# Kernel tuning notes

Hardware: AMD Instinct MI355X
Metric: run time of the kernel (lower is better)

## Reference

```python
import jax, jax.numpy as jnp
import numpy as np

N_NODES = 50000
N_EDGES = 800000
D_NODE = 128
D_EDGE = 16
HID = 128
BN_EPS = 1e-5


def gcn_conv(h, src, dst, W, b):
    # PyG GCNConv: h' = D^-1/2 (A + I) D^-1/2 (h W) + b, deg includes self-loop
    h = h @ W
    deg = jax.ops.segment_sum(jnp.ones((src.shape[0],), h.dtype), dst,
                              num_segments=N_NODES) + 1.0
    dinv = deg ** -0.5
    norm = dinv[src] * dinv[dst]                      # [E]
    agg = jax.ops.segment_sum(h[src] * norm[:, None], dst,
                              num_segments=N_NODES)   # scatter to dst
    agg = agg + h * (dinv * dinv)[:, None]            # self-loop term
    return agg + b


def setup_inputs() -> dict:
    key = jax.random.key(0)
    ks = jax.random.split(key, 12)
    s = lambda fan_in: 1.0 / np.sqrt(fan_in)
    return {
        "x": jax.random.normal(ks[0], (N_NODES, D_NODE), jnp.float32),
        "edge_index": jax.random.randint(ks[1], (2, N_EDGES), 0, N_NODES, jnp.int32),
        "edge_attr": jax.random.normal(ks[2], (N_EDGES, D_EDGE), jnp.float32),
        "W1": jax.random.normal(ks[3], (D_NODE, HID), jnp.float32) * s(D_NODE),
        "b1": jnp.zeros((HID,), jnp.float32),
        "gamma": jnp.ones((HID,), jnp.float32),
        "beta": jnp.zeros((HID,), jnp.float32),
        "W2": jax.random.normal(ks[4], (HID, HID), jnp.float32) * s(HID),
        "b2": jnp.zeros((HID,), jnp.float32),
        "Wm1": jax.random.normal(ks[5], (2 * HID + D_EDGE, HID), jnp.float32) * s(2 * HID + D_EDGE),
        "bm1": jnp.zeros((HID,), jnp.float32),
        "Wm2": jax.random.normal(ks[6], (HID, 1), jnp.float32) * s(HID),
        "bm2": jnp.zeros((1,), jnp.float32),
    }


def reference(x, edge_index, edge_attr, W1, b1, gamma, beta, W2, b2, Wm1, bm1, Wm2, bm2):
    src, dst = edge_index[0], edge_index[1]
    z = gcn_conv(x, src, dst, W1, b1)
    # BatchNorm1d over nodes (training-mode batch stats, biased var)
    mean = jnp.mean(z, axis=0)
    var = jnp.mean(jnp.square(z - mean), axis=0)
    z = (z - mean) * jax.lax.rsqrt(var + BN_EPS) * gamma + beta
    z = jax.nn.relu(z)
    z = gcn_conv(z, src, dst, W2, b2)
    # edge head: gather endpoints, concat with edge_attr, 2-layer MLP (dropout = eval identity)
    edge_input = jnp.concatenate([z[src], z[dst], edge_attr], axis=1)  # [E, 2H+De]
    h = jax.nn.relu(edge_input @ Wm1 + bm1)
    return (h @ Wm2 + bm2).squeeze(-1)  # [E]
```

## Files before the change

kernel.cpp:

```cpp
#include <hip/hip_runtime.h>
#include <hip/hip_bf16.h>

#define NN 50000
#define NE 800000
#define H 128
#define DE 16
#define BN_EPS 1e-5f
#define NB_SCAN 196

typedef float v2f __attribute__((ext_vector_type(2)));
typedef float v4f __attribute__((ext_vector_type(4)));
typedef short bfrag __attribute__((ext_vector_type(8)));

__device__ __forceinline__ unsigned int packbf2(float a, float b) {
    __hip_bfloat162 h = __float22bfloat162_rn(make_float2(a, b));
    return *(unsigned int*)&h;
}
__device__ __forceinline__ v2f unpackbf2(unsigned int u) {
    v2f r;
    r.x = __uint_as_float(u << 16);
    r.y = __uint_as_float(u & 0xffff0000u);
    return r;
}
__device__ __forceinline__ bfrag cvt8(float4 a0, float4 a1) {
    union { uint4 u; bfrag f; } x;
    x.u.x = packbf2(a0.x, a0.y);
    x.u.y = packbf2(a0.z, a0.w);
    x.u.z = packbf2(a1.x, a1.y);
    x.u.w = packbf2(a1.z, a1.w);
    return x.f;
}
__device__ __forceinline__ bfrag cvt8v(v4f a0, v4f a1) {
    union { uint4 u; bfrag f; } x;
    x.u.x = packbf2(a0.x, a0.y);
    x.u.y = packbf2(a0.z, a0.w);
    x.u.z = packbf2(a1.x, a1.y);
    x.u.w = packbf2(a1.z, a1.w);
    return x.f;
}
#define COMP(u4, j) ((j) == 0 ? (u4).x : (j) == 1 ? (u4).y : (j) == 2 ? (u4).z : (u4).w)

__global__ void hist_k(const int* __restrict__ dst, int* __restrict__ counts) {
    int e = blockIdx.x * 256 + threadIdx.x;
    if (e < NE) atomicAdd(&counts[dst[e]], 1);
}

__global__ void scan1_k(const int* __restrict__ counts, int* __restrict__ bsum) {
    __shared__ int sh[256];
    int i = blockIdx.x * 256 + threadIdx.x;
    int v = (i < NN) ? counts[i] : 0;
    sh[threadIdx.x] = v;
    __syncthreads();
    for (int off = 128; off; off >>= 1) {
        if (threadIdx.x < off) sh[threadIdx.x] += sh[threadIdx.x + off];
        __syncthreads();
    }
    if (!threadIdx.x) bsum[blockIdx.x] = sh[0];
}

__global__ void scan2_k(int* __restrict__ bsum) {
    __shared__ int sh[256];
    int t = threadIdx.x;
    int v = (t < NB_SCAN) ? bsum[t] : 0;
    sh[t] = v;
    __syncthreads();
    for (int off = 1; off < 256; off <<= 1) {
        int x = (t >= off) ? sh[t - off] : 0;
        __syncthreads();
        sh[t] += x;
        __syncthreads();
    }
    if (t < NB_SCAN) bsum[t] = sh[t] - v;
}

__global__ void scan3_k(const int* __restrict__ counts, const int* __restrict__ bsum,
                        int* __restrict__ offsets, int* __restrict__ cursor,
                        float* __restrict__ dinv) {
    __shared__ int sh[256];
    int i = blockIdx.x * 256 + threadIdx.x;
    int v = (i < NN) ? counts[i] : 0;
    sh[threadIdx.x] = v;
    __syncthreads();
    for (int off = 1; off < 256; off <<= 1) {
        int x = (threadIdx.x >= off) ? sh[threadIdx.x - off] : 0;
        __syncthreads();
        sh[threadIdx.x] += x;
        __syncthreads();
    }
    if (i < NN) {
        int excl = sh[threadIdx.x] - v + bsum[blockIdx.x];
        offsets[i] = excl;
        cursor[i] = excl;
        dinv[i] = rsqrtf((float)v + 1.0f);
    }
}

__global__ void fill_k(const int* __restrict__ src, const int* __restrict__ dst,
                       int* __restrict__ cursor, int* __restrict__ srcs) {
    int e = blockIdx.x * 256 + threadIdx.x;
    if (e < NE) {
        int d = dst[e];
        int pos = atomicAdd(&cursor[d], 1);
        srcs[pos] = src[e];
    }
}

__global__ void cvtB_k(const float* __restrict__ s0, const float* __restrict__ s1,
                       const float* __restrict__ s2, const float* __restrict__ s3,
                       short* __restrict__ d0, short* __restrict__ d1,
                       short* __restrict__ d2, short* __restrict__ d3) {
    const float* s = blockIdx.y == 0 ? s0 : blockIdx.y == 1 ? s1 : blockIdx.y == 2 ? s2 : s3;
    short* d = blockIdx.y == 0 ? d0 : blockIdx.y == 1 ? d1 : blockIdx.y == 2 ? d2 : d3;
    int idx = blockIdx.x * 256 + threadIdx.x;
    int n = idx & 127, k = idx >> 7;
    float v = s[k * 128 + n];
    d[n * 128 + k] = (short)(packbf2(v, v) & 0xffff);
}

__global__ void cvtWe_k(const float* __restrict__ We, unsigned int* __restrict__ WePk) {
    int idx = blockIdx.x * 256 + threadIdx.x;
    if (idx < 2048) {
        int c = idx >> 8;
        int lane = (idx >> 2) & 63;
        int j2 = (idx & 3) * 2;
        int q = lane >> 4, i = lane & 15;
        int k0 = q * 8 + j2, k1 = k0 + 1;
        int feat = i * 8 + c;
        float v0 = (k0 < 16) ? We[k0 * 128 + feat] : 0.f;
        float v1 = (k1 < 16) ? We[k1 * 128 + feat] : 0.f;
        WePk[idx] = packbf2(v0, v1);
    }
}

__global__ __launch_bounds__(256) void gemm_mfma(const float* __restrict__ A,
                                                 const short* __restrict__ Bt,
                                                 float* __restrict__ C,
                                                 unsigned int* __restrict__ Cb,
                                                 const float* __restrict__ rowScale,
                                                 const float* __restrict__ tA,
                                                 const float* __restrict__ tC,
                                                 int M) {
    int lane = threadIdx.x & 63;
    int w = threadIdx.x >> 6;
    int i = lane & 15;
    int q = lane >> 4;
    int r0 = blockIdx.x * 64 + w * 16;
    int arow = min(r0 + i, M - 1);
    const float* Arow = A + (size_t)arow * 128;

    v4f acc[8];
#pragma unroll
    for (int c = 0; c < 8; c++) acc[c] = (v4f)0.f;

#pragma unroll
    for (int kc = 0; kc < 128; kc += 32) {
        int kb = kc + q * 8;
        float4 a0 = *(const float4*)&Arow[kb];
        float4 a1 = *(const float4*)&Arow[kb + 4];
        if (tA) {
            float4 t0 = *(const float4*)&tA[kb];
            float4 t1 = *(const float4*)&tA[kb + 4];
            float4 c0 = *(const float4*)&tC[kb];
            float4 c1 = *(const float4*)&tC[kb + 4];
            a0.x = fmaxf(a0.x * t0.x + c0.x, 0.f);
            a0.y = fmaxf(a0.y * t0.y + c0.y, 0.f);
            a0.z = fmaxf(a0.z * t0.z + c0.z, 0.f);
            a0.w = fmaxf(a0.w * t0.w + c0.w, 0.f);
            a1.x = fmaxf(a1.x * t1.x + c1.x, 0.f);
            a1.y = fmaxf(a1.y * t1.y + c1.y, 0.f);
            a1.z = fmaxf(a1.z * t1.z + c1.z, 0.f);
            a1.w = fmaxf(a1.w * t1.w + c1.w, 0.f);
        }
        bfrag af = cvt8(a0, a1);
#pragma unroll
        for (int c = 0; c < 8; c++) {
            bfrag bf = *(const bfrag*)&Bt[(size_t)(c * 16 + i) * 128 + kb];
            acc[c] = __builtin_amdgcn_mfma_f32_16x16x32_bf16(af, bf, acc[c], 0, 0, 0);
        }
    }

    int orow0 = r0 + q * 4;
    v4f ds = (v4f)1.f;
    if (rowScale) ds = *(const v4f*)&rowScale[min(orow0, M - 4)];
    if (Cb) {
#pragma unroll
        for (int c = 0; c < 8; c++) {
            int col = c * 16 + i;
#pragma unroll
            for (int r = 0; r < 4; r++) {
                float v = acc[c][r] * ds[r];
                float vp = __shfl_xor(v, 1, 64);
                if (!(i & 1) && orow0 + r < M)
                    Cb[(size_t)(orow0 + r) * 64 + (col >> 1)] = packbf2(v, vp);
            }
        }
    } else {
#pragma unroll
        for (int c = 0; c < 8; c++) {
            int col = c * 16 + i;
#pragma unroll
            for (int r = 0; r < 4; r++) {
                if (orow0 + r < M)
                    C[(size_t)(orow0 + r) * 128 + col] = acc[c][r] * ds[r];
            }
        }
    }
}

__global__ __launch_bounds__(256) void gemm_pq(const unsigned int* __restrict__ zbA,
                                               const short* __restrict__ Bs_,
                                               const short* __restrict__ Bd_,
                                               const float* __restrict__ bm1,
                                               unsigned int* __restrict__ Pb,
                                               unsigned int* __restrict__ Qb,
                                               int M) {
    int lane = threadIdx.x & 63;
    int w = threadIdx.x >> 6;
    int i = lane & 15;
    int q = lane >> 4;
    int r0 = blockIdx.x * 64 + w * 16;
    int arow = min(r0 + i, M - 1);

    v4f accP[8], accQ[8];
#pragma unroll
    for (int c = 0; c < 8; c++) { accP[c] = (v4f)0.f; accQ[c] = (v4f)0.f; }

#pragma unroll
    for (int kc = 0; kc < 128; kc += 32) {
        int kb = kc + q * 8;
        bfrag af = *(const bfrag*)&zbA[(size_t)arow * 64 + (kb >> 1)];
#pragma unroll
        for (int c = 0; c < 8; c++) {
            bfrag bs = *(const bfrag*)&Bs_[(size_t)(c * 16 + i) * 128 + kb];
            bfrag bd = *(const bfrag*)&Bd_[(size_t)(c * 16 + i) * 128 + kb];
            accP[c] = __builtin_amdgcn_mfma_f32_16x16x32_bf16(af, bs, accP[c], 0, 0, 0);
            accQ[c] = __builtin_amdgcn_mfma_f32_16x16x32_bf16(af, bd, accQ[c], 0, 0, 0);
        }
    }

    int orow0 = r0 + q * 4;
    float bm1c[8];
#pragma unroll
    for (int c = 0; c < 8; c++) bm1c[c] = bm1[c * 16 + i];
#pragma unroll
    for (int c = 0; c < 8; c++) {
        int col = c * 16 + i;
#pragma unroll
        for (int r = 0; r < 4; r++) {
            float vP = accP[c][r];
            float vPp = __shfl_xor(vP, 1, 64);
            float vQ = accQ[c][r] + bm1c[c];
            float vQp = __shfl_xor(vQ, 1, 64);
            if (!(i & 1) && orow0 + r < M) {
                Pb[(size_t)(orow0 + r) * 64 + (col >> 1)] = packbf2(vP, vPp);
                Qb[(size_t)(orow0 + r) * 64 + (col >> 1)] = packbf2(vQ, vQp);
            }
        }
    }
}

__global__ __launch_bounds__(256, 8) void aggregate_k(const unsigned int* __restrict__ hsb,
                                                      const int* __restrict__ offsets,
                                                      const int* __restrict__ counts,
                                                      const int* __restrict__ srcs,
                                                      const float* __restrict__ dinv,
                                                      const float* __restrict__ bias,
                                                      float* __restrict__ zout,
                                                      unsigned int* __restrict__ zbout) {
    int lane = threadIdx.x & 63;
    int n = __builtin_amdgcn_readfirstlane(blockIdx.x * 4 + (threadIdx.x >> 6));
    if (n >= NN) return;
    int beg = offsets[n];
    int cnt = counts[n];
    v2f a0 = {0.f, 0.f}, a1 = {0.f, 0.f}, a2 = {0.f, 0.f}, a3 = {0.f, 0.f};
    v2f a4 = {0.f, 0.f}, a5 = {0.f, 0.f}, a6 = {0.f, 0.f}, a7 = {0.f, 0.f};
    for (int c = 0; c < cnt; c += 64) {
        int vsrc = srcs[beg + c + lane];
        int m = min(64, cnt - c);
        int t = 0;
        for (; t + 8 <= m; t += 8) {
            int s0 = __builtin_amdgcn_readlane(vsrc, t);
            int s1 = __builtin_amdgcn_readlane(vsrc, t + 1);
            int s2 = __builtin_amdgcn_readlane(vsrc, t + 2);
            int s3 = __builtin_amdgcn_readlane(vsrc, t + 3);
            int s4 = __builtin_amdgcn_readlane(vsrc, t + 4);
            int s5 = __builtin_amdgcn_readlane(vsrc, t + 5);
            int s6 = __builtin_amdgcn_readlane(vsrc, t + 6);
            int s7 = __builtin_amdgcn_readlane(vsrc, t + 7);
            unsigned int u0 = hsb[(size_t)s0 * 64 + lane];
            unsigned int u1 = hsb[(size_t)s1 * 64 + lane];
            unsigned int u2 = hsb[(size_t)s2 * 64 + lane];
            unsigned int u3 = hsb[(size_t)s3 * 64 + lane];
            unsigned int u4 = hsb[(size_t)s4 * 64 + lane];
            unsigned int u5 = hsb[(size_t)s5 * 64 + lane];
            unsigned int u6 = hsb[(size_t)s6 * 64 + lane];
            unsigned int u7 = hsb[(size_t)s7 * 64 + lane];
            a0 += unpackbf2(u0);
            a1 += unpackbf2(u1);
            a2 += unpackbf2(u2);
            a3 += unpackbf2(u3);
            a4 += unpackbf2(u4);
            a5 += unpackbf2(u5);
            a6 += unpackbf2(u6);
            a7 += unpackbf2(u7);
        }
        for (; t < m; t++) {
            int s0 = __builtin_amdgcn_readlane(vsrc, t);
            a0 += unpackbf2(hsb[(size_t)s0 * 64 + lane]);
        }
    }
    v2f self = unpackbf2(hsb[(size_t)n * 64 + lane]);
    float di = dinv[n];
    int f = lane * 2;
    float2 b = *(const float2*)&bias[f];
    v2f sum = ((a0 + a1) + (a2 + a3)) + ((a4 + a5) + (a6 + a7)) + self;
    float rx = sum.x * di + b.x;
    float ry = sum.y * di + b.y;
    if (zbout) {
        zbout[(size_t)n * 64 + lane] = packbf2(rx, ry);
    } else {
        *(float2*)&zout[(size_t)n * 128 + f] = make_float2(rx, ry);
    }
}

__global__ __launch_bounds__(256) void bnstats_k(const float* __restrict__ z,
                                                 float* __restrict__ sums,
                                                 float* __restrict__ sumsq) {
    __shared__ float ls[128], lq[128];
    int f = threadIdx.x & 127;
    int sub = threadIdx.x >> 7;
    float s = 0.f, q = 0.f;
    for (int r = blockIdx.x * 2 + sub; r < NN; r += gridDim.x * 2) {
        float v = z[(size_t)r * 128 + f];
        s += v;
        q += v * v;
    }
    if (sub) { ls[f] = s; lq[f] = q; }
    __syncthreads();
    if (!sub) {
        atomicAdd(&sums[f], s + ls[f]);
        atomicAdd(&sumsq[f], q + lq[f]);
    }
}

__global__ void bnfinal_k(const float* __restrict__ sums, const float* __restrict__ sumsq,
                          const float* __restrict__ gamma, const float* __restrict__ beta,
                          float* __restrict__ bnA, float* __restrict__ bnC) {
    int f = threadIdx.x;
    if (f < 128) {
        float mean = sums[f] * (1.0f / NN);
        float var = sumsq[f] * (1.0f / NN) - mean * mean;
        float a = gamma[f] * rsqrtf(var + BN_EPS);
        bnA[f] = a;
        bnC[f] = beta[f] - mean * a;
    }
}

__global__ __launch_bounds__(256) void edgehead_k(const unsigned int* __restrict__ Pb,
                                                  const unsigned int* __restrict__ Qb,
                                                  const float* __restrict__ ea,
                                                  const int* __restrict__ srcI,
                                                  const int* __restrict__ dstI,
                                                  const unsigned int* __restrict__ WePk,
                                                  const float* __restrict__ Wm2,
                                                  const float* __restrict__ bm2,
                                                  float* __restrict__ out) {
    int lane = threadIdx.x & 63;
    int wid = threadIdx.x >> 6;
    int base = (blockIdx.x * 4 + wid) * 64;
    int i = lane & 15;
    int q = lane >> 4;

    bfrag wef[8];
#pragma unroll
    for (int c = 0; c < 8; c++)
        wef[c] = *(const bfrag*)&WePk[(c * 64 + lane) * 4];
    float4 wv0 = *(const float4*)&Wm2[i * 8];
    float4 wv1 = *(const float4*)&Wm2[i * 8 + 4];
    float bm2v = bm2[0];

    int sv = srcI[base + lane];
    int dv = dstI[base + lane];

#pragma unroll
    for (int t = 0; t < 4; t++) {
        int tb = t * 16;
        bfrag af;
#pragma unroll
        for (int z = 0; z < 8; z++) af[z] = 0;
        if (q < 2) {
            const float* erow = &ea[(size_t)(base + tb + i) * 16 + q * 8];
            v4f e0 = __builtin_nontemporal_load((const v4f*)erow);
            v4f e1 = __builtin_nontemporal_load((const v4f*)(erow + 4));
            af = cvt8v(e0, e1);
        }
        uint4 Pu[4], Qu[4];
#pragma unroll
        for (int r = 0; r < 4; r++) {
            int sr = __shfl(sv, tb + q * 4 + r, 64);
            int dr = __shfl(dv, tb + q * 4 + r, 64);
            Pu[r] = *(const uint4*)&Pb[(size_t)sr * 64 + i * 4];
            Qu[r] = *(const uint4*)&Qb[(size_t)dr * 64 + i * 4];
        }
        v4f acc[8];
#pragma unroll
        for (int c = 0; c < 8; c++) acc[c] = (v4f)0.f;
#pragma unroll
        for (int c = 0; c < 8; c++)
            acc[c] = __builtin_amdgcn_mfma_f32_16x16x32_bf16(af, wef[c], acc[c], 0, 0, 0);
        float wvp[8] = {wv0.x, wv0.y, wv0.z, wv0.w, wv1.x, wv1.y, wv1.z, wv1.w};
#pragma unroll
        for (int r = 0; r < 4; r++) {
            float s = 0.f;
#pragma unroll
            for (int j = 0; j < 4; j++) {
                v2f pv = unpackbf2(COMP(Pu[r], j));
                v2f qv = unpackbf2(COMP(Qu[r], j));
                float t0 = acc[2 * j][r] + pv.x + qv.x;
                float t1 = acc[2 * j + 1][r] + pv.y + qv.y;
                t0 = fmaxf(t0, 0.f);
                t1 = fmaxf(t1, 0.f);
                s = fmaf(t0, wvp[2 * j], s);
                s = fmaf(t1, wvp[2 * j + 1], s);
            }
#pragma unroll
            for (int off = 1; off <= 8; off <<= 1) s += __shfl_xor(s, off, 64);
            if (i == 0) __builtin_nontemporal_store(s + bm2v, &out[base + tb + q * 4 + r]);
        }
    }
}

extern "C" void kernel_launch(void* const* d_in, const int* in_sizes, int n_in,
                              void* d_out, int out_size, void* d_ws, size_t ws_size,
                              hipStream_t stream) {
    const float* x     = (const float*)d_in[0];
    const int*   ei    = (const int*)d_in[1];
    const float* ea    = (const float*)d_in[2];
    const float* W1    = (const float*)d_in[3];
    const float* b1    = (const float*)d_in[4];
    const float* gamma = (const float*)d_in[5];
    const float* beta  = (const float*)d_in[6];
    const float* W2    = (const float*)d_in[7];
    const float* b2    = (const float*)d_in[8];
    const float* Wm1   = (const float*)d_in[9];
    const float* bm1   = (const float*)d_in[10];
    const float* Wm2   = (const float*)d_in[11];
    const float* bm2   = (const float*)d_in[12];
    float* out = (float*)d_out;

    const int* srcI = ei;
    const int* dstI = ei + NE;

    char* w = (char*)d_ws;
    auto alloc = [&](size_t bytes) {
        char* p = w;
        w += (bytes + 255) & ~(size_t)255;
        return p;
    };
    float* dinv    = (float*)alloc(NN * 4);
    int*   counts  = (int*)alloc(NN * 4);
    int*   offsets = (int*)alloc(NN * 4);
    int*   cursor  = (int*)alloc(NN * 4);
    int*   bsum    = (int*)alloc(256 * 4);
    int*   srcs    = (int*)alloc((size_t)(NE + 64) * 4);
    float* sums    = (float*)alloc(128 * 4);
    float* sumsq   = (float*)alloc(128 * 4);
    float* bnA     = (float*)alloc(128 * 4);
    float* bnC     = (float*)alloc(128 * 4);
    short* bt1     = (short*)alloc(128 * 128 * 2);
    short* bt2     = (short*)alloc(128 * 128 * 2);
    short* bts     = (short*)alloc(128 * 128 * 2);
    short* btd     = (short*)alloc(128 * 128 * 2);
    unsigned int* WePk = (unsigned int*)alloc(2048 * 4);
    unsigned int* hsb  = (unsigned int*)alloc((size_t)NN * 64 * 4);
    float* bufZ    = (float*)alloc((size_t)NN * 128 * 4);
    unsigned int* zb2 = (unsigned int*)bufZ;
    unsigned int* Qb  = (unsigned int*)bufZ + (size_t)NN * 64;

    hipMemsetAsync(counts, 0, NN * 4, stream);
    hipMemsetAsync(sums, 0, 128 * 4, stream);
    hipMemsetAsync(sumsq, 0, 128 * 4, stream);

    hist_k<<<(NE + 255) / 256, 256, 0, stream>>>(dstI, counts);
    scan1_k<<<NB_SCAN, 256, 0, stream>>>(counts, bsum);
    scan2_k<<<1, 256, 0, stream>>>(bsum);
    scan3_k<<<NB_SCAN, 256, 0, stream>>>(counts, bsum, offsets, cursor, dinv);
    fill_k<<<(NE + 255) / 256, 256, 0, stream>>>(srcI, dstI, cursor, srcs);
    cvtB_k<<<dim3(64, 4), 256, 0, stream>>>(W1, W2, Wm1, Wm1 + 128 * 128,
                                            bt1, bt2, bts, btd);
    cvtWe_k<<<8, 256, 0, stream>>>(Wm1 + 256 * 128, WePk);

    const int GB = (NN + 63) / 64;
    const int AGG = (NN + 3) / 4;

    gemm_mfma<<<GB, 256, 0, stream>>>(x, bt1, nullptr, hsb, dinv, nullptr, nullptr, NN);
    aggregate_k<<<AGG, 256, 0, stream>>>(hsb, offsets, counts, srcs, dinv, b1, bufZ, nullptr);

    bnstats_k<<<256, 256, 0, stream>>>(bufZ, sums, sumsq);
    bnfinal_k<<<1, 128, 0, stream>>>(sums, sumsq, gamma, beta, bnA, bnC);

    gemm_mfma<<<GB, 256, 0, stream>>>(bufZ, bt2, nullptr, hsb, dinv, bnA, bnC, NN);
    aggregate_k<<<AGG, 256, 0, stream>>>(hsb, offsets, counts, srcs, dinv, b2, nullptr, zb2);

    gemm_pq<<<GB, 256, 0, stream>>>(zb2, bts, btd, bm1, hsb, Qb, NN);

    edgehead_k<<<NE / 256, 256, 0, stream>>>(hsb, Qb, ea, srcI, dstI, WePk,
                                             Wm2, bm2, out);
}
```

Measured before the change: 463.5 us.

## Store first-layer GCN output in bf16 and fuse weight conversion kernels

Stores the first aggregation output as packed bf16 rather than fp32. BN statistics and the second GEMM's fused BN+ReLU prologue now read the bf16 buffer, which halves that intermediate's traffic. The two weight-conversion kernels are merged into one launch, and the edge-head reduction switches from shuffles to DPP row reductions with packed v2f math. The cost is some loss of precision in the BN statistics and the layer-2 input.

```diff
diff --git a/kernel.cpp b/kernel.cpp
--- a/kernel.cpp
+++ b/kernel.cpp
@@ -39,6 +39,14 @@
     return x.f;
 }
 #define COMP(u4, j) ((j) == 0 ? (u4).x : (j) == 1 ? (u4).y : (j) == 2 ? (u4).z : (u4).w)
+
+__device__ __forceinline__ float dpp_rowred16(float s) {
+    s += __int_as_float(__builtin_amdgcn_update_dpp(0, __float_as_int(s), 0x121, 0xf, 0xf, false));
+    s += __int_as_float(__builtin_amdgcn_update_dpp(0, __float_as_int(s), 0x122, 0xf, 0xf, false));
+    s += __int_as_float(__builtin_amdgcn_update_dpp(0, __float_as_int(s), 0x124, 0xf, 0xf, false));
+    s += __int_as_float(__builtin_amdgcn_update_dpp(0, __float_as_int(s), 0x128, 0xf, 0xf, false));
+    return s;
+}
 
 __global__ void hist_k(const int* __restrict__ dst, int* __restrict__ counts) {
     int e = blockIdx.x * 256 + threadIdx.x;
@@ -105,21 +113,23 @@
     }
 }
 
-__global__ void cvtB_k(const float* __restrict__ s0, const float* __restrict__ s1,
-                       const float* __restrict__ s2, const float* __restrict__ s3,
-                       short* __restrict__ d0, short* __restrict__ d1,
-                       short* __restrict__ d2, short* __restrict__ d3) {
-    const float* s = blockIdx.y == 0 ? s0 : blockIdx.y == 1 ? s1 : blockIdx.y == 2 ? s2 : s3;
-    short* d = blockIdx.y == 0 ? d0 : blockIdx.y == 1 ? d1 : blockIdx.y == 2 ? d2 : d3;
-    int idx = blockIdx.x * 256 + threadIdx.x;
-    int n = idx & 127, k = idx >> 7;
-    float v = s[k * 128 + n];
-    d[n * 128 + k] = (short)(packbf2(v, v) & 0xffff);
-}
-
-__global__ void cvtWe_k(const float* __restrict__ We, unsigned int* __restrict__ WePk) {
-    int idx = blockIdx.x * 256 + threadIdx.x;
-    if (idx < 2048) {
+__global__ void cvtAll_k(const float* __restrict__ W1, const float* __restrict__ W2,
+                         const float* __restrict__ Ws, const float* __restrict__ Wd,
+                         const float* __restrict__ We,
+                         short* __restrict__ d1, short* __restrict__ d2,
+                         short* __restrict__ ds_, short* __restrict__ dd,
+                         unsigned int* __restrict__ WePk) {
+    int b = blockIdx.x;
+    if (b < 256) {
+        int mat = b >> 6;
+        const float* s = mat == 0 ? W1 : mat == 1 ? W2 : mat == 2 ? Ws : Wd;
+        short* d = mat == 0 ? d1 : mat == 1 ? d2 : mat == 2 ? ds_ : dd;
+        int idx = (b & 63) * 256 + threadIdx.x;
+        int n = idx & 127, k = idx >> 7;
+        float v = s[k * 128 + n];
+        d[n * 128 + k] = (short)(packbf2(v, v) & 0xffff);
+    } else {
+        int idx = (b - 256) * 256 + threadIdx.x;
         int c = idx >> 8;
         int lane = (idx >> 2) & 63;
         int j2 = (idx & 3) * 2;
@@ -133,8 +143,8 @@
 }
 
 __global__ __launch_bounds__(256) void gemm_mfma(const float* __restrict__ A,
+                                                 const unsigned int* __restrict__ Ab,
                                                  const short* __restrict__ Bt,
-                                                 float* __restrict__ C,
                                                  unsigned int* __restrict__ Cb,
                                                  const float* __restrict__ rowScale,
                                                  const float* __restrict__ tA,
@@ -146,7 +156,6 @@
     int q = lane >> 4;
     int r0 = blockIdx.x * 64 + w * 16;
     int arow = min(r0 + i, M - 1);
-    const float* Arow = A + (size_t)arow * 128;
 
     v4f acc[8];
 #pragma unroll
@@ -155,23 +164,29 @@
 #pragma unroll
     for (int kc = 0; kc < 128; kc += 32) {
         int kb = kc + q * 8;
-        float4 a0 = *(const float4*)&Arow[kb];
-        float4 a1 = *(const float4*)&Arow[kb + 4];
-        if (tA) {
-            float4 t0 = *(const float4*)&tA[kb];
-            float4 t1 = *(const float4*)&tA[kb + 4];
-            float4 c0 = *(const float4*)&tC[kb];
-            float4 c1 = *(const float4*)&tC[kb + 4];
-            a0.x = fmaxf(a0.x * t0.x + c0.x, 0.f);
-            a0.y = fmaxf(a0.y * t0.y + c0.y, 0.f);
-            a0.z = fmaxf(a0.z * t0.z + c0.z, 0.f);
-            a0.w = fmaxf(a0.w * t0.w + c0.w, 0.f);
-            a1.x = fmaxf(a1.x * t1.x + c1.x, 0.f);
-            a1.y = fmaxf(a1.y * t1.y + c1.y, 0.f);
-            a1.z = fmaxf(a1.z * t1.z + c1.z, 0.f);
-            a1.w = fmaxf(a1.w * t1.w + c1.w, 0.f);
-        }
-        bfrag af = cvt8(a0, a1);
+        bfrag af;
+        if (Ab) {
+            uint4 u = *(const uint4*)&Ab[(size_t)arow * 64 + (kb >> 1)];
+            v2f z0 = unpackbf2(u.x), z1 = unpackbf2(u.y);
+            v2f z2 = unpackbf2(u.z), z3 = unpackbf2(u.w);
+            v2f t0 = *(const v2f*)&tA[kb],     c0 = *(const v2f*)&tC[kb];
+            v2f t1 = *(const v2f*)&tA[kb + 2], c1 = *(const v2f*)&tC[kb + 2];
+            v2f t2 = *(const v2f*)&tA[kb + 4], c2 = *(const v2f*)&tC[kb + 4];
+            v2f t3 = *(const v2f*)&tA[kb + 6], c3 = *(const v2f*)&tC[kb + 6];
+            z0 = z0 * t0 + c0; z1 = z1 * t1 + c1;
+            z2 = z2 * t2 + c2; z3 = z3 * t3 + c3;
+            union { uint4 u; bfrag f; } x;
+            x.u.x = packbf2(fmaxf(z0.x, 0.f), fmaxf(z0.y, 0.f));
+            x.u.y = packbf2(fmaxf(z1.x, 0.f), fmaxf(z1.y, 0.f));
+            x.u.z = packbf2(fmaxf(z2.x, 0.f), fmaxf(z2.y, 0.f));
+            x.u.w = packbf2(fmaxf(z3.x, 0.f), fmaxf(z3.y, 0.f));
+            af = x.f;
+        } else {
+            const float* Arow = A + (size_t)arow * 128;
+            float4 a0 = *(const float4*)&Arow[kb];
+            float4 a1 = *(const float4*)&Arow[kb + 4];
+            af = cvt8(a0, a1);
+        }
 #pragma unroll
         for (int c = 0; c < 8; c++) {
             bfrag bf = *(const bfrag*)&Bt[(size_t)(c * 16 + i) * 128 + kb];
@@ -182,27 +197,15 @@
     int orow0 = r0 + q * 4;
     v4f ds = (v4f)1.f;
     if (rowScale) ds = *(const v4f*)&rowScale[min(orow0, M - 4)];
-    if (Cb) {
-#pragma unroll
-        for (int c = 0; c < 8; c++) {
-            int col = c * 16 + i;
-#pragma unroll
-            for (int r = 0; r < 4; r++) {
-                float v = acc[c][r] * ds[r];
-                float vp = __shfl_xor(v, 1, 64);
-                if (!(i & 1) && orow0 + r < M)
-                    Cb[(size_t)(orow0 + r) * 64 + (col >> 1)] = packbf2(v, vp);
-            }
-        }
-    } else {
-#pragma unroll
-        for (int c = 0; c < 8; c++) {
-            int col = c * 16 + i;
-#pragma unroll
-            for (int r = 0; r < 4; r++) {
-                if (orow0 + r < M)
-                    C[(size_t)(orow0 + r) * 128 + col] = acc[c][r] * ds[r];
-            }
+#pragma unroll
+    for (int c = 0; c < 8; c++) {
+        int col = c * 16 + i;
+#pragma unroll
+        for (int r = 0; r < 4; r++) {
+            float v = acc[c][r] * ds[r];
+            float vp = __shfl_xor(v, 1, 64);
+            if (!(i & 1) && orow0 + r < M)
+                Cb[(size_t)(orow0 + r) * 64 + (col >> 1)] = packbf2(v, vp);
         }
     }
 }
@@ -323,23 +326,27 @@
     }
 }
 
-__global__ __launch_bounds__(256) void bnstats_k(const float* __restrict__ z,
-                                                 float* __restrict__ sums,
-                                                 float* __restrict__ sumsq) {
-    __shared__ float ls[128], lq[128];
-    int f = threadIdx.x & 127;
-    int sub = threadIdx.x >> 7;
-    float s = 0.f, q = 0.f;
-    for (int r = blockIdx.x * 2 + sub; r < NN; r += gridDim.x * 2) {
-        float v = z[(size_t)r * 128 + f];
+__global__ __launch_bounds__(256) void bnstats_b_k(const unsigned int* __restrict__ zb,
+                                                   float* __restrict__ sums,
+                                                   float* __restrict__ sumsq) {
+    __shared__ v2f ls[4][64], lq[4][64];
+    int lane = threadIdx.x & 63;
+    int sub = threadIdx.x >> 6;
+    v2f s = {0.f, 0.f}, q = {0.f, 0.f};
+    for (int r = blockIdx.x * 4 + sub; r < NN; r += gridDim.x * 4) {
+        v2f v = unpackbf2(zb[(size_t)r * 64 + lane]);
         s += v;
         q += v * v;
     }
-    if (sub) { ls[f] = s; lq[f] = q; }
+    if (sub) { ls[sub][lane] = s; lq[sub][lane] = q; }
     __syncthreads();
     if (!sub) {
-        atomicAdd(&sums[f], s + ls[f]);
-        atomicAdd(&sumsq[f], q + lq[f]);
+        s += ls[1][lane] + ls[2][lane] + ls[3][lane];
+        q += lq[1][lane] + lq[2][lane] + lq[3][lane];
+        atomicAdd(&sums[lane * 2], s.x);
+        atomicAdd(&sums[lane * 2 + 1], s.y);
+        atomicAdd(&sumsq[lane * 2], q.x);
+        atomicAdd(&sumsq[lane * 2 + 1], q.y);
     }
 }
 
@@ -377,6 +384,11 @@
         wef[c] = *(const bfrag*)&WePk[(c * 64 + lane) * 4];
     float4 wv0 = *(const float4*)&Wm2[i * 8];
     float4 wv1 = *(const float4*)&Wm2[i * 8 + 4];
+    v2f wv2[4];
+    wv2[0].x = wv0.x; wv2[0].y = wv0.y;
+    wv2[1].x = wv0.z; wv2[1].y = wv0.w;
+    wv2[2].x = wv1.x; wv2[2].y = wv1.y;
+    wv2[3].x = wv1.z; wv2[3].y = wv1.w;
     float bm2v = bm2[0];
 
     int sv = srcI[base + lane];
@@ -408,23 +420,20 @@
 #pragma unroll
         for (int c = 0; c < 8; c++)
             acc[c] = __builtin_amdgcn_mfma_f32_16x16x32_bf16(af, wef[c], acc[c], 0, 0, 0);
-        float wvp[8] = {wv0.x, wv0.y, wv0.z, wv0.w, wv1.x, wv1.y, wv1.z, wv1.w};
 #pragma unroll
         for (int r = 0; r < 4; r++) {
-            float s = 0.f;
+            v2f sa = {0.f, 0.f};
 #pragma unroll
             for (int j = 0; j < 4; j++) {
-                v2f pv = unpackbf2(COMP(Pu[r], j));
-                v2f qv = unpackbf2(COMP(Qu[r], j));
-                float t0 = acc[2 * j][r] + pv.x + qv.x;
-                float t1 = acc[2 * j + 1][r] + pv.y + qv.y;
-                t0 = fmaxf(t0, 0.f);
-                t1 = fmaxf(t1, 0.f);
-                s = fmaf(t0, wvp[2 * j], s);
-                s = fmaf(t1, wvp[2 * j + 1], s);
+                v2f pq = unpackbf2(COMP(Pu[r], j)) + unpackbf2(COMP(Qu[r], j));
+                v2f tt;
+                tt.x = acc[2 * j][r] + pq.x;
+                tt.y = acc[2 * j + 1][r] + pq.y;
+                tt.x = fmaxf(tt.x, 0.f);
+                tt.y = fmaxf(tt.y, 0.f);
+                sa += tt * wv2[j];
             }
-#pragma unroll
-            for (int off = 1; off <= 8; off <<= 1) s += __shfl_xor(s, off, 64);
+            float s = dpp_rowred16(sa.x + sa.y);
             if (i == 0) __builtin_nontemporal_store(s + bm2v, &out[base + tb + q * 4 + r]);
         }
     }
@@ -473,9 +482,9 @@
     short* btd     = (short*)alloc(128 * 128 * 2);
     unsigned int* WePk = (unsigned int*)alloc(2048 * 4);
     unsigned int* hsb  = (unsigned int*)alloc((size_t)NN * 64 * 4);
-    float* bufZ    = (float*)alloc((size_t)NN * 128 * 4);
-    unsigned int* zb2 = (unsigned int*)bufZ;
-    unsigned int* Qb  = (unsigned int*)bufZ + (size_t)NN * 64;
+    unsigned int* zb1  = (unsigned int*)alloc((size_t)NN * 64 * 4);
+    unsigned int* Qb   = (unsigned int*)alloc((size_t)NN * 64 * 4);
+    unsigned int* zb2  = zb1;
 
     hipMemsetAsync(counts, 0, NN * 4, stream);
     hipMemsetAsync(sums, 0, 128 * 4, stream);
@@ -486,20 +495,19 @@
     scan2_k<<<1, 256, 0, stream>>>(bsum);
     scan3_k<<<NB_SCAN, 256, 0, stream>>>(counts, bsum, offsets, cursor, dinv);
     fill_k<<<(NE + 255) / 256, 256, 0, stream>>>(srcI, dstI, cursor, srcs);
-    cvtB_k<<<dim3(64, 4), 256, 0, stream>>>(W1, W2, Wm1, Wm1 + 128 * 128,
-                                            bt1, bt2, bts, btd);
-    cvtWe_k<<<8, 256, 0, stream>>>(Wm1 + 256 * 128, WePk);
+    cvtAll_k<<<264, 256, 0, stream>>>(W1, W2, Wm1, Wm1 + 128 * 128, Wm1 + 256 * 128,
+                                      bt1, bt2, bts, btd, WePk);
 
     const int GB = (NN + 63) / 64;
     const int AGG = (NN + 3) / 4;
 
-    gemm_mfma<<<GB, 256, 0, stream>>>(x, bt1, nullptr, hsb, dinv, nullptr, nullptr, NN);
-    aggregate_k<<<AGG, 256, 0, stream>>>(hsb, offsets, counts, srcs, dinv, b1, bufZ, nullptr);
-
-    bnstats_k<<<256, 256, 0, stream>>>(bufZ, sums, sumsq);
+    gemm_mfma<<<GB, 256, 0, stream>>>(x, nullptr, bt1, hsb, dinv, nullptr, nullptr, NN);
+    aggregate_k<<<AGG, 256, 0, stream>>>(hsb, offsets, counts, srcs, dinv, b1, nullptr, zb1);
+
+    bnstats_b_k<<<256, 256, 0, stream>>>(zb1, sums, sumsq);
     bnfinal_k<<<1, 128, 0, stream>>>(sums, sumsq, gamma, beta, bnA, bnC);
 
-    gemm_mfma<<<GB, 256, 0, stream>>>(bufZ, bt2, nullptr, hsb, dinv, bnA, bnC, NN);
+    gemm_mfma<<<GB, 256, 0, stream>>>(nullptr, zb1, bt2, hsb, dinv, bnA, bnC, NN);
     aggregate_k<<<AGG, 256, 0, stream>>>(hsb, offsets, counts, srcs, dinv, b2, nullptr, zb2);
 
     gemm_pq<<<GB, 256, 0, stream>>>(zb2, bts, btd, bm1, hsb, Qb, NN);
```

Result: faster. 448.4 us (-3.3%).
